# Kernel tuning notes

Measured on AMD Instinct MI355X. Metric: run time of the kernel, lower is better.

Reference implementation:

```python
import jax, jax.numpy as jnp
import numpy as np

N, D, DFF, E, F, K, H = 4096, 512, 512, 512, 4096, 1024, 4


def _rn(i, shape, s=0.02):
    return jax.random.normal(jax.random.fold_in(jax.random.key(0), i), shape, dtype=jnp.float32) * s


def setup_inputs():
    inp = {"inputs": jax.random.normal(jax.random.key(1), (N, D), dtype=jnp.float32)}
    i = 10
    for p in ("enc", "dec"):
        for nm, shp in (("wq", (D, D)), ("wk", (D, D)), ("wv", (D, D)), ("wo", (D, D)), ("w1", (D, DFF)), ("w2", (DFF, D))):
            inp[p + "_" + nm] = _rn(i, shp); i += 1
        for nm, shp in (("bq", (D,)), ("bk", (D,)), ("bv", (D,)), ("bo", (D,)), ("b1", (DFF,)), ("b2", (D,))):
            inp[p + "_" + nm] = jnp.zeros(shp, jnp.float32)
        inp[p + "_ln1_g"] = jnp.ones((D,), jnp.float32)
        inp[p + "_ln1_b"] = jnp.zeros((D,), jnp.float32)
        inp[p + "_ln2_g"] = jnp.ones((D,), jnp.float32)
        inp[p + "_ln2_b"] = jnp.zeros((D,), jnp.float32)
    inp["fc1_w"] = _rn(100, (D, E))
    inp["fc1_b"] = jnp.zeros((E,), jnp.float32)
    inp["fc2_w"] = _rn(101, (D, F))
    inp["fc2_b"] = jnp.zeros((F,), jnp.float32)
    inp["emb"] = _rn(102, (K, E), s=0.01)
    return inp


def layer_norm(x, g, b, eps=1e-6):
    mu = jnp.mean(x, axis=-1, keepdims=True)
    var = jnp.mean(jnp.square(x - mu), axis=-1, keepdims=True)
    return (x - mu) * jax.lax.rsqrt(var + eps) * g + b


def row_distance(a, b):
    # cosine similarity between rows (sim in [-1,1]; loss maps (sim+1)/2 -> [0,1])
    an = a * jax.lax.rsqrt(jnp.maximum(jnp.sum(a * a, axis=1, keepdims=True), 1e-12))
    bn = b * jax.lax.rsqrt(jnp.maximum(jnp.sum(b * b, axis=1, keepdims=True), 1e-12))
    return an @ bn.T


def nearest_context(feature, context):
    distances = row_distance(feature, context) * -1.0  # [N, K]
    min_ind = jnp.argmin(distances, axis=1)
    one_hot = jax.nn.one_hot(min_ind, context.shape[0], dtype=jnp.float32)  # [N, K]
    rslt = one_hot @ jax.lax.stop_gradient(context)  # [N, E]
    return rslt, one_hot


@jax.custom_vjp
def vq(feature, context):
    return nearest_context(feature, context)[0]


def _vq_fwd(feature, context):
    value, ind = nearest_context(feature, context)
    return value, ind


def _vq_bwd(ind, d_value):
    # straight-through to feature, scatter-add (via one-hot matmul) to codebook
    return d_value, ind.T @ d_value


vq.defvjp(_vq_fwd, _vq_bwd)


def encoder_layer(x, wq, bq, wk, bk, wv, bv, wo, bo, w1, b1, w2, b2, g1, be1, g2, be2):
    n, d = x.shape
    dh = d // H
    q = (x @ wq + bq).reshape(n, H, dh)
    k = (x @ wk + bk).reshape(n, H, dh)
    v = (x @ wv + bv).reshape(n, H, dh)
    scores = jnp.einsum('nhd,mhd->hnm', q, k) / jnp.sqrt(jnp.float32(dh))
    attn = jax.nn.softmax(scores, axis=-1)
    ctx = jnp.einsum('hnm,mhd->nhd', attn, v).reshape(n, d)
    out1 = layer_norm(x + (ctx @ wo + bo), g1, be1)
    ffn = jax.nn.relu(out1 @ w1 + b1) @ w2 + b2
    return layer_norm(out1 + ffn, g2, be2)


def reference(inputs, enc_wq, enc_wk, enc_wv, enc_wo, enc_w1, enc_w2, enc_bq, enc_bk, enc_bv, enc_bo, enc_b1, enc_b2, enc_ln1_g, enc_ln1_b, enc_ln2_g, enc_ln2_b, dec_wq, dec_wk, dec_wv, dec_wo, dec_w1, dec_w2, dec_bq, dec_bk, dec_bv, dec_bo, dec_b1, dec_b2, dec_ln1_g, dec_ln1_b, dec_ln2_g, dec_ln2_b, fc1_w, fc1_b, fc2_w, fc2_b, emb):
    encoded = encoder_layer(inputs, enc_wq, enc_bq, enc_wk, enc_bk, enc_wv, enc_bv, enc_wo, enc_bo, enc_w1, enc_b1, enc_w2, enc_b2, enc_ln1_g, enc_ln1_b, enc_ln2_g, enc_ln2_b)
    encoded = encoded @ fc1_w + fc1_b  # [N, E]
    vq_feat = vq(encoded, emb)
    _, context_ind = nearest_context(encoded, emb)
    decoded = encoder_layer(vq_feat, dec_wq, dec_bq, dec_wk, dec_bk, dec_wv, dec_bv, dec_wo, dec_bo, dec_w1, dec_b1, dec_w2, dec_b2, dec_ln1_g, dec_ln1_b, dec_ln2_g, dec_ln2_b)
    decoded = jax.nn.relu(decoded @ fc2_w + fc2_b)  # [N, F]
    return encoded, vq_feat, context_ind, decoded, emb
```

## Files before the change

kernel.cpp:

```cpp
#include <hip/hip_runtime.h>
#include <hip/hip_bf16.h>
#include <stdint.h>

typedef __bf16 bf16;
typedef __bf16 bf16x8 __attribute__((ext_vector_type(8)));
typedef float  f32x4v __attribute__((ext_vector_type(4)));

__device__ __forceinline__ void cvt8(const float* v, bf16x8& hh, bf16x8& ll) {
    #pragma unroll
    for (int j = 0; j < 8; j++) {
        bf16 b = (bf16)v[j]; hh[j] = b; ll[j] = (bf16)(v[j] - (float)b);
    }
}

__device__ __forceinline__ float block_reduce_sum256(float v) {
    __shared__ float red[256];
    int tid = threadIdx.x;
    red[tid] = v; __syncthreads();
    #pragma unroll
    for (int s = 128; s > 0; s >>= 1) {
        if (tid < s) red[tid] += red[tid + s];
        __syncthreads();
    }
    float r = red[0]; __syncthreads();
    return r;
}

template<int BMT, bool RELU, bool TRANS, bool BNAT, bool HILO>
__global__ __launch_bounds__(256, 2)
void gemm3(const float* __restrict__ A, const float* __restrict__ B,
           const float* __restrict__ bias, float* __restrict__ C,
           bf16* __restrict__ Chi, bf16* __restrict__ Clo,
           int K, int lda, int ldb, int ldc, float alpha)
{
    constexpr int BN = 128, TK = 32;
    constexpr int RM = BMT / 32;
    __shared__ __align__(16) bf16 Ah[BMT * TK];
    __shared__ __align__(16) bf16 Al[BMT * TK];
    __shared__ __align__(16) bf16 Bh[BN * TK];
    __shared__ __align__(16) bf16 Bl[BN * TK];

    const int tid  = threadIdx.x;
    const int wave = tid >> 6, lane = tid & 63;
    const int wr = wave >> 1, wc = wave & 1;
    const long bm = (long)blockIdx.y * BMT;
    const long bn = (long)blockIdx.x * BN;
    const int fr = lane & 15, fq = lane >> 4;

    f32x4v acc[RM][4] = {};

    for (int k0 = 0; k0 < K; k0 += TK) {
        #pragma unroll
        for (int it = 0; it < BMT / 64; it++) {
            const int c = it * 256 + tid;
            const int r = c >> 2, k8 = c & 3;
            const float* src = A + (bm + r) * (long)lda + k0 + k8 * 8;
            float4 f0 = ((const float4*)src)[0], f1 = ((const float4*)src)[1];
            float v[8] = {f0.x, f0.y, f0.z, f0.w, f1.x, f1.y, f1.z, f1.w};
            bf16x8 hh, ll; cvt8(v, hh, ll);
            *(bf16x8*)&Ah[r * TK + k8 * 8] = hh;
            *(bf16x8*)&Al[r * TK + k8 * 8] = ll;
        }
        if (BNAT) {
            const int col = tid & 127, bkh = (tid >> 7) * 16;
            const float* src = B + (long)(k0 + bkh) * ldb + bn + col;
            float v[16];
            #pragma unroll
            for (int kk = 0; kk < 16; kk++) v[kk] = src[(long)kk * ldb];
            bf16x8 h0, l0, h1, l1; cvt8(v, h0, l0); cvt8(v + 8, h1, l1);
            bf16* hd = &Bh[col * TK + bkh];
            bf16* ld_ = &Bl[col * TK + bkh];
            ((bf16x8*)hd)[0] = h0; ((bf16x8*)hd)[1] = h1;
            ((bf16x8*)ld_)[0] = l0; ((bf16x8*)ld_)[1] = l1;
        } else {
            #pragma unroll
            for (int it = 0; it < 2; it++) {
                const int c = it * 256 + tid;
                const int r = c >> 2, k8 = c & 3;
                const float* src = B + (bn + r) * (long)ldb + k0 + k8 * 8;
                float4 f0 = ((const float4*)src)[0], f1 = ((const float4*)src)[1];
                float v[8] = {f0.x, f0.y, f0.z, f0.w, f1.x, f1.y, f1.z, f1.w};
                bf16x8 hh, ll; cvt8(v, hh, ll);
                *(bf16x8*)&Bh[r * TK + k8 * 8] = hh;
                *(bf16x8*)&Bl[r * TK + k8 * 8] = ll;
            }
        }
        __syncthreads();

        bf16x8 ah[RM], am[RM], bh[4], bm_[4];
        #pragma unroll
        for (int i = 0; i < RM; i++) {
            const int r = (wr * (BMT / 2) + i * 16 + fr) * TK + fq * 8;
            ah[i] = *(const bf16x8*)&Ah[r];
            am[i] = *(const bf16x8*)&Al[r];
        }
        #pragma unroll
        for (int j = 0; j < 4; j++) {
            const int r = (wc * 64 + j * 16 + fr) * TK + fq * 8;
            bh[j] = *(const bf16x8*)&Bh[r];
            bm_[j] = *(const bf16x8*)&Bl[r];
        }
        #pragma unroll
        for (int i = 0; i < RM; i++)
            #pragma unroll
            for (int j = 0; j < 4; j++) {
                acc[i][j] = __builtin_amdgcn_mfma_f32_16x16x32_bf16(am[i], bh[j], acc[i][j], 0, 0, 0);
                acc[i][j] = __builtin_amdgcn_mfma_f32_16x16x32_bf16(ah[i], bm_[j], acc[i][j], 0, 0, 0);
                acc[i][j] = __builtin_amdgcn_mfma_f32_16x16x32_bf16(ah[i], bh[j], acc[i][j], 0, 0, 0);
            }
        __syncthreads();
    }

    #pragma unroll
    for (int i = 0; i < RM; i++) {
        #pragma unroll
        for (int j = 0; j < 4; j++) {
            const long col = bn + wc * 64 + j * 16 + fr;
            const float bv = bias ? bias[col] : 0.f;
            #pragma unroll
            for (int r = 0; r < 4; r++) {
                const long row = bm + wr * (BMT / 2) + i * 16 + fq * 4 + r;
                float v = acc[i][j][r] * alpha + bv;
                if (RELU) v = fmaxf(v, 0.f);
                const long idx = TRANS ? (col * (long)ldc + row) : (row * (long)ldc + col);
                if (HILO) {
                    bf16 hh = (bf16)v;
                    Chi[idx] = hh;
                    Clo[idx] = (bf16)(v - (float)hh);
                } else {
                    C[idx] = v;
                }
            }
        }
    }
}

__global__ __launch_bounds__(256, 2)
void qkv_gemm(const float* __restrict__ X,
              const float* __restrict__ Wq, const float* __restrict__ Wk, const float* __restrict__ Wv,
              const float* __restrict__ Bq, const float* __restrict__ Bk, const float* __restrict__ Bv,
              float* __restrict__ Qo, bf16* __restrict__ Khi, bf16* __restrict__ Klo,
              bf16* __restrict__ Vthi, bf16* __restrict__ Vtlo)
{
    constexpr int TK = 32, D = 512, N = 4096;
    __shared__ __align__(16) bf16 Ah[64 * TK];
    __shared__ __align__(16) bf16 Al[64 * TK];
    __shared__ __align__(16) bf16 Bh[128 * TK];
    __shared__ __align__(16) bf16 Bl[128 * TK];

    const int tid  = threadIdx.x;
    const int wave = tid >> 6, lane = tid & 63;
    const int wr = wave >> 1, wc = wave & 1;
    const int sel = blockIdx.x >> 2, wcol0 = (blockIdx.x & 3) * 128;
    const long bm = (long)blockIdx.y * 64;
    const int fr = lane & 15, fq = lane >> 4;

    const float* W  = sel == 0 ? Wq : (sel == 1 ? Wk : Wv);
    const float* Bb = sel == 0 ? Bq : (sel == 1 ? Bk : Bv);

    f32x4v acc[2][4] = {};

    for (int k0 = 0; k0 < D; k0 += TK) {
        {
            const int r = tid >> 2, k8 = tid & 3;
            const float* src = X + (bm + r) * (long)D + k0 + k8 * 8;
            float4 f0 = ((const float4*)src)[0], f1 = ((const float4*)src)[1];
            float v[8] = {f0.x, f0.y, f0.z, f0.w, f1.x, f1.y, f1.z, f1.w};
            bf16x8 hh, ll; cvt8(v, hh, ll);
            *(bf16x8*)&Ah[r * TK + k8 * 8] = hh;
            *(bf16x8*)&Al[r * TK + k8 * 8] = ll;
        }
        {
            const int col = tid & 127, bkh = (tid >> 7) * 16;
            const float* src = W + (long)(k0 + bkh) * D + wcol0 + col;
            float v[16];
            #pragma unroll
            for (int kk = 0; kk < 16; kk++) v[kk] = src[(long)kk * D];
            bf16x8 h0, l0, h1, l1; cvt8(v, h0, l0); cvt8(v + 8, h1, l1);
            bf16* hd = &Bh[col * TK + bkh];
            bf16* ld_ = &Bl[col * TK + bkh];
            ((bf16x8*)hd)[0] = h0; ((bf16x8*)hd)[1] = h1;
            ((bf16x8*)ld_)[0] = l0; ((bf16x8*)ld_)[1] = l1;
        }
        __syncthreads();

        bf16x8 ah[2], am[2], bh[4], bm_[4];
        #pragma unroll
        for (int i = 0; i < 2; i++) {
            const int r = (wr * 32 + i * 16 + fr) * TK + fq * 8;
            ah[i] = *(const bf16x8*)&Ah[r];
            am[i] = *(const bf16x8*)&Al[r];
        }
        #pragma unroll
        for (int j = 0; j < 4; j++) {
            const int r = (wc * 64 + j * 16 + fr) * TK + fq * 8;
            bh[j] = *(const bf16x8*)&Bh[r];
            bm_[j] = *(const bf16x8*)&Bl[r];
        }
        #pragma unroll
        for (int i = 0; i < 2; i++)
            #pragma unroll
            for (int j = 0; j < 4; j++) {
                acc[i][j] = __builtin_amdgcn_mfma_f32_16x16x32_bf16(am[i], bh[j], acc[i][j], 0, 0, 0);
                acc[i][j] = __builtin_amdgcn_mfma_f32_16x16x32_bf16(ah[i], bm_[j], acc[i][j], 0, 0, 0);
                acc[i][j] = __builtin_amdgcn_mfma_f32_16x16x32_bf16(ah[i], bh[j], acc[i][j], 0, 0, 0);
            }
        __syncthreads();
    }

    #pragma unroll
    for (int i = 0; i < 2; i++) {
        #pragma unroll
        for (int j = 0; j < 4; j++) {
            const int col = wc * 64 + j * 16 + fr;
            const float bv = Bb[wcol0 + col];
            #pragma unroll
            for (int r = 0; r < 4; r++) {
                const long row = bm + wr * 32 + i * 16 + fq * 4 + r;
                const float v = acc[i][j][r] + bv;
                if (sel == 0) {
                    Qo[row * D + wcol0 + col] = v;
                } else {
                    const bf16 hh = (bf16)v;
                    const bf16 ll = (bf16)(v - (float)hh);
                    const long idx = (sel == 1) ? (row * (long)D + wcol0 + col)
                                                : ((long)(wcol0 + col) * N + row);
                    if (sel == 1) { Khi[idx] = hh; Klo[idx] = ll; }
                    else          { Vthi[idx] = hh; Vtlo[idx] = ll; }
                }
            }
        }
    }
}

__global__ __launch_bounds__(256, 4)
void flash_attn(const float* __restrict__ Q,
                const bf16* __restrict__ Khi, const bf16* __restrict__ Klo,
                const bf16* __restrict__ Vthi, const bf16* __restrict__ Vtlo,
                float* __restrict__ Op, float* __restrict__ ml)
{
    constexpr int N = 4096, D = 512, SPAN = 1024, TKV = 32, NT = SPAN / TKV;
    constexpr float TS = 0.12751791f;

    __shared__ __align__(16) bf16 smem[16384];
    bf16* Kh = smem;
    bf16* Kl = smem + 4096;
    bf16* Vh = smem + 8192;
    bf16* Vl = smem + 12288;

    const int tid = threadIdx.x;
    const int wave = tid >> 6, lane = tid & 63;
    const int fr = lane & 15, fq = lane >> 4;
    const int qt = blockIdx.x, h = blockIdx.y, s = blockIdx.z;
    const long q0 = (long)qt * 64;

    const int kn = tid >> 4, kk8 = tid & 15;
    const int vd = tid >> 2, vk8 = tid & 3;
    const int kof0 = kn * 128 + ((kk8 ^ (kn & 15)) << 3);
    const int kof1 = (kn + 16) * 128 + ((kk8 ^ ((kn + 16) & 15)) << 3);
    const int vof0 = vd * 32 + ((vk8 ^ ((vd >> 2) & 3)) << 3);
    const int vof1 = (vd + 64) * 32 + ((vk8 ^ (((vd + 64) >> 2) & 3)) << 3);

    bf16x8 qh[4], ql[4];
    #pragma unroll
    for (int kt = 0; kt < 4; kt++) {
        const float* src = Q + (q0 + wave * 16 + fr) * D + h * 128 + kt * 32 + fq * 8;
        float4 f0 = ((const float4*)src)[0], f1 = ((const float4*)src)[1];
        float v[8] = {f0.x, f0.y, f0.z, f0.w, f1.x, f1.y, f1.z, f1.w};
        cvt8(v, qh[kt], ql[kt]);
    }

    f32x4v o[8] = {};
    float m_run = -1e30f, l_run = 0.f;

    const int j0base = s * SPAN;

    #pragma unroll 1
    for (int jt = 0; jt < NT; jt++) {
        const int j0 = j0base + jt * TKV;

        {
            const long kg0 = (long)(j0 + kn) * D + h * 128 + kk8 * 8;
            const long kg1 = (long)(j0 + kn + 16) * D + h * 128 + kk8 * 8;
            const long vg0 = (long)(h * 128 + vd) * N + j0 + vk8 * 8;
            const long vg1 = (long)(h * 128 + vd + 64) * N + j0 + vk8 * 8;
            uint4 a0 = *(const uint4*)&Khi[kg0], a1 = *(const uint4*)&Klo[kg0];
            uint4 a2 = *(const uint4*)&Khi[kg1], a3 = *(const uint4*)&Klo[kg1];
            uint4 b0 = *(const uint4*)&Vthi[vg0], b1 = *(const uint4*)&Vtlo[vg0];
            uint4 b2 = *(const uint4*)&Vthi[vg1], b3 = *(const uint4*)&Vtlo[vg1];
            *(uint4*)&Kh[kof0] = a0; *(uint4*)&Kl[kof0] = a1;
            *(uint4*)&Kh[kof1] = a2; *(uint4*)&Kl[kof1] = a3;
            *(uint4*)&Vh[vof0] = b0; *(uint4*)&Vl[vof0] = b1;
            *(uint4*)&Vh[vof1] = b2; *(uint4*)&Vl[vof1] = b3;
        }
        __syncthreads();

        f32x4v sacc[2] = {};
        #pragma unroll
        for (int jb = 0; jb < 2; jb++) {
            bf16x8 kh[4], km[4];
            #pragma unroll
            for (int kt = 0; kt < 4; kt++) {
                const int off = (jb * 16 + fr) * 128 + (((kt * 4 + fq) ^ fr) << 3);
                kh[kt] = *(const bf16x8*)&Kh[off];
                km[kt] = *(const bf16x8*)&Kl[off];
            }
            __builtin_amdgcn_s_setprio(1);
            #pragma unroll
            for (int kt = 0; kt < 4; kt++) {
                sacc[jb] = __builtin_amdgcn_mfma_f32_16x16x32_bf16(km[kt], qh[kt], sacc[jb], 0, 0, 0);
                sacc[jb] = __builtin_amdgcn_mfma_f32_16x16x32_bf16(kh[kt], ql[kt], sacc[jb], 0, 0, 0);
                sacc[jb] = __builtin_amdgcn_mfma_f32_16x16x32_bf16(kh[kt], qh[kt], sacc[jb], 0, 0, 0);
            }
            __builtin_amdgcn_s_setprio(0);
        }

        float t[2][4];
        float mloc = -1e30f;
        #pragma unroll
        for (int jb = 0; jb < 2; jb++)
            #pragma unroll
            for (int r = 0; r < 4; r++) {
                t[jb][r] = sacc[jb][r] * TS;
                mloc = fmaxf(mloc, t[jb][r]);
            }
        mloc = fmaxf(mloc, __shfl_xor(mloc, 16));
        mloc = fmaxf(mloc, __shfl_xor(mloc, 32));
        const float mn = fmaxf(m_run, mloc);
        const float alpha = exp2f(m_run - mn);
        m_run = mn;

        float p[2][4];
        float rs = 0.f;
        #pragma unroll
        for (int jb = 0; jb < 2; jb++)
            #pragma unroll
            for (int r = 0; r < 4; r++) {
                p[jb][r] = exp2f(t[jb][r] - mn);
                rs += p[jb][r];
            }
        rs += __shfl_xor(rs, 16);
        rs += __shfl_xor(rs, 32);
        l_run = l_run * alpha + rs;

        unsigned int hp[2][2], lp[2][2];
        #pragma unroll
        for (int jb = 0; jb < 2; jb++)
            #pragma unroll
            for (int t2 = 0; t2 < 2; t2++) {
                const float p0 = p[jb][2 * t2], p1 = p[jb][2 * t2 + 1];
                const bf16 h0 = (bf16)p0, h1 = (bf16)p1;
                const unsigned short u0 = __builtin_bit_cast(unsigned short, h0);
                const unsigned short u1 = __builtin_bit_cast(unsigned short, h1);
                hp[jb][t2] = (unsigned int)u0 | ((unsigned int)u1 << 16);
                const bf16 g0 = (bf16)(p0 - (float)h0), g1 = (bf16)(p1 - (float)h1);
                const unsigned short w0 = __builtin_bit_cast(unsigned short, g0);
                const unsigned short w1 = __builtin_bit_cast(unsigned short, g1);
                lp[jb][t2] = (unsigned int)w0 | ((unsigned int)w1 << 16);
            }

        uint4 PH, PL;
        {
            unsigned int phw[4], plw[4];
            #pragma unroll
            for (int w = 0; w < 4; w++) {
                const int src = ((2 * (fq & 1) + (w >> 1)) << 4) + fr;
                const unsigned int h0 = (unsigned int)__shfl((int)hp[0][w & 1], src);
                const unsigned int h1 = (unsigned int)__shfl((int)hp[1][w & 1], src);
                phw[w] = (fq >> 1) ? h1 : h0;
                const unsigned int g0 = (unsigned int)__shfl((int)lp[0][w & 1], src);
                const unsigned int g1 = (unsigned int)__shfl((int)lp[1][w & 1], src);
                plw[w] = (fq >> 1) ? g1 : g0;
            }
            PH.x = phw[0]; PH.y = phw[1]; PH.z = phw[2]; PH.w = phw[3];
            PL.x = plw[0]; PL.y = plw[1]; PL.z = plw[2]; PL.w = plw[3];
        }
        const bf16x8 ph = __builtin_bit_cast(bf16x8, PH);
        const bf16x8 pl = __builtin_bit_cast(bf16x8, PL);

        float alr[4];
        #pragma unroll
        for (int r = 0; r < 4; r++) alr[r] = __shfl(alpha, fq * 4 + r);
        #pragma unroll
        for (int jbo = 0; jbo < 8; jbo++)
            #pragma unroll
            for (int r = 0; r < 4; r++)
                o[jbo][r] *= alr[r];

        #pragma unroll
        for (int jbo = 0; jbo < 8; jbo++) {
            const int off = (jbo * 16 + fr) * 32 + ((fq ^ ((fr >> 2) & 3)) << 3);
            const bf16x8 vh_ = *(const bf16x8*)&Vh[off];
            const bf16x8 vl_ = *(const bf16x8*)&Vl[off];
            __builtin_amdgcn_s_setprio(1);
            o[jbo] = __builtin_amdgcn_mfma_f32_16x16x32_bf16(pl, vh_, o[jbo], 0, 0, 0);
            o[jbo] = __builtin_amdgcn_mfma_f32_16x16x32_bf16(ph, vl_, o[jbo], 0, 0, 0);
            o[jbo] = __builtin_amdgcn_mfma_f32_16x16x32_bf16(ph, vh_, o[jbo], 0, 0, 0);
            __builtin_amdgcn_s_setprio(0);
        }
        __syncthreads();
    }

    const long sidx = (long)((h * 64 + qt) * 4 + s);
    float* ob = Op + sidx * 8192;
    #pragma unroll
    for (int jbo = 0; jbo < 8; jbo++)
        #pragma unroll
        for (int r = 0; r < 4; r++) {
            const int lrow = wave * 16 + fq * 4 + r;
            ob[lrow * 128 + jbo * 16 + fr] = o[jbo][r];
        }
    if (fq == 0) {
        const int lrow = wave * 16 + fr;
        ml[sidx * 128 + lrow]      = m_run;
        ml[sidx * 128 + 64 + lrow] = l_run;
    }
}

__global__ void flash_merge(const float* __restrict__ Op, const float* __restrict__ ml,
                            float* __restrict__ ctx)
{
    const int idx = blockIdx.x;
    const int h = idx >> 6, qt = idx & 63;
    const int tid = threadIdx.x;
    __shared__ float es[4][64], il[64];
    if (tid < 64) {
        float m[4], l[4];
        #pragma unroll
        for (int s = 0; s < 4; s++) {
            m[s] = ml[(long)(idx * 4 + s) * 128 + tid];
            l[s] = ml[(long)(idx * 4 + s) * 128 + 64 + tid];
        }
        float mx = fmaxf(fmaxf(m[0], m[1]), fmaxf(m[2], m[3]));
        float denom = 0.f;
        #pragma unroll
        for (int s = 0; s < 4; s++) {
            const float e = exp2f(m[s] - mx);
            es[s][tid] = e;
            denom += e * l[s];
        }
        il[tid] = 1.f / denom;
    }
    __syncthreads();
    const long b = (long)idx * 4 * 8192;
    #pragma unroll
    for (int i = 0; i < 32; i++) {
        const int e = tid + i * 256;
        const int row = e >> 7, col = e & 127;
        float v = es[0][row] * Op[b + e] + es[1][row] * Op[b + 8192 + e]
                + es[2][row] * Op[b + 16384 + e] + es[3][row] * Op[b + 24576 + e];
        ctx[(long)(qt * 64 + row) * 512 + h * 128 + col] = v * il[row];
    }
}

__global__ void add_ln_f32(const float* __restrict__ a, const float* __restrict__ b,
                           const float* __restrict__ g, const float* __restrict__ be,
                           float* __restrict__ out)
{
    const long row = blockIdx.x;
    const int tid = threadIdx.x;
    const long base = row * 512L;
    float x0 = a[base + tid]       + b[base + tid];
    float x1 = a[base + tid + 256] + b[base + tid + 256];
    float s = block_reduce_sum256(x0 + x1);
    float mu = s * (1.f / 512.f);
    float d0 = x0 - mu, d1 = x1 - mu;
    float var = block_reduce_sum256(d0 * d0 + d1 * d1) * (1.f / 512.f);
    float invs = rsqrtf(var + 1e-6f);
    out[base + tid]       = d0 * invs * g[tid]       + be[tid];
    out[base + tid + 256] = d1 * invs * g[tid + 256] + be[tid + 256];
}

__global__ void normalize_emb(const float* __restrict__ emb, float* __restrict__ embn)
{
    const long row = blockIdx.x;
    const int tid = threadIdx.x;
    const long base = row * 512L;
    float a0 = emb[base + tid];
    float a1 = emb[base + tid + 256];
    float ss = block_reduce_sum256(a0 * a0 + a1 * a1);
    float sc = rsqrtf(fmaxf(ss, 1e-12f));
    embn[base + tid]       = a0 * sc;
    embn[base + tid + 256] = a1 * sc;
}

__global__ void vq_select_onehot(float* __restrict__ sims, const float* __restrict__ emb,
                                 float* __restrict__ vq_out)
{
    __shared__ float sv[256];
    __shared__ int   si[256];
    const long row = blockIdx.x;
    const int tid = threadIdx.x;
    float* s = sims + row * 1024L;
    float v0 = s[tid], v1 = s[tid + 256], v2 = s[tid + 512], v3 = s[tid + 768];
    float best = v0; int bi = tid;
    if (v1 > best) { best = v1; bi = tid + 256; }
    if (v2 > best) { best = v2; bi = tid + 512; }
    if (v3 > best) { best = v3; bi = tid + 768; }
    sv[tid] = best; si[tid] = bi; __syncthreads();
    #pragma unroll
    for (int st = 128; st > 0; st >>= 1) {
        if (tid < st) {
            if (sv[tid + st] > sv[tid] ||
                (sv[tid + st] == sv[tid] && si[tid + st] < si[tid])) {
                sv[tid] = sv[tid + st]; si[tid] = si[tid + st];
            }
        }
        __syncthreads();
    }
    const int idx = si[0];
    s[tid]       = (tid       == idx) ? 1.f : 0.f;
    s[tid + 256] = (tid + 256 == idx) ? 1.f : 0.f;
    s[tid + 512] = (tid + 512 == idx) ? 1.f : 0.f;
    s[tid + 768] = (tid + 768 == idx) ? 1.f : 0.f;
    const float* er = emb + (long)idx * 512;
    float* vr = vq_out + row * 512L;
    vr[tid]       = er[tid];
    vr[tid + 256] = er[tid + 256];
}

struct EncW {
    const float *wq, *wk, *wv, *wo, *w1, *w2;
    const float *bq, *bk, *bv, *bo, *b1, *b2;
    const float *g1, *be1, *g2, *be2;
};

static void run_encoder_g3(hipStream_t stream, const float* x, const EncW& w,
                           float* qb, bf16* khi, bf16* klo, bf16* vthi, bf16* vtlo,
                           float* ctx, float* Op, float* ml,
                           float* x1, float* hb, float* out)
{
    const int N = 4096, D = 512;
    qkv_gemm<<<dim3(12, 64), 256, 0, stream>>>(
        x, w.wq, w.wk, w.wv, w.bq, w.bk, w.bv, qb, khi, klo, vthi, vtlo);
    flash_attn<<<dim3(64, 4, 4), 256, 0, stream>>>(qb, khi, klo, vthi, vtlo, Op, ml);
    flash_merge<<<256, 256, 0, stream>>>(Op, ml, ctx);
    gemm3<64, false, false, true, false><<<dim3(4, 64), 256, 0, stream>>>(
        ctx, w.wo, w.bo, qb, nullptr, nullptr, D, D, D, D, 1.f);
    add_ln_f32<<<N, 256, 0, stream>>>(x, qb, w.g1, w.be1, x1);
    gemm3<64, true, false, true, false><<<dim3(4, 64), 256, 0, stream>>>(
        x1, w.w1, w.b1, hb, nullptr, nullptr, D, D, D, D, 1.f);
    gemm3<64, false, false, true, false><<<dim3(4, 64), 256, 0, stream>>>(
        hb, w.w2, w.b2, qb, nullptr, nullptr, D, D, D, D, 1.f);
    add_ln_f32<<<N, 256, 0, stream>>>(x1, qb, w.g2, w.be2, out);
}

extern "C" void kernel_launch(void* const* d_in, const int* in_sizes, int n_in,
                              void* d_out, int out_size, void* d_ws, size_t ws_size,
                              hipStream_t stream)
{
    const int N = 4096, D = 512, E = 512, F = 4096, KCB = 1024;
    (void)in_sizes; (void)n_in; (void)out_size; (void)d_ws; (void)ws_size;

    const float* x_in  = (const float*)d_in[0];
    const float* fc1_w = (const float*)d_in[33];
    const float* fc1_b = (const float*)d_in[34];
    const float* fc2_w = (const float*)d_in[35];
    const float* fc2_b = (const float*)d_in[36];
    const float* emb   = (const float*)d_in[37];

    float* out0 = (float*)d_out;
    float* out1 = out0 + (size_t)N * E;
    float* out2 = out1 + (size_t)N * E;
    float* out3 = out2 + (size_t)N * KCB;
    float* out4 = out3 + (size_t)N * F;

    char* arena = (char*)out3;
    const size_t MB = 1024 * 1024;
    float* qb     = (float*)(arena + 0 * MB);
    bf16*  khi    = (bf16*) (arena + 8 * MB);
    bf16*  klo    = (bf16*) (arena + 12 * MB);
    bf16*  vthi   = (bf16*) (arena + 16 * MB);
    bf16*  vtlo   = (bf16*) (arena + 20 * MB);
    float* ctx    = (float*)(arena + 24 * MB);
    float* Op     = (float*)(arena + 32 * MB);
    float* decout = (float*)(arena + 56 * MB);
    float* x1     = (float*)(arena + 16 * MB);
    float* hb     = (float*)(arena + 8 * MB);
    float* ml     = (float*)out4;
    float* embn   = out1;
    float* stage  = (float*)out4;

    EncW ew = { (const float*)d_in[1],  (const float*)d_in[2],  (const float*)d_in[3],
                (const float*)d_in[4],  (const float*)d_in[5],  (const float*)d_in[6],
                (const float*)d_in[7],  (const float*)d_in[8],  (const float*)d_in[9],
                (const float*)d_in[10], (const float*)d_in[11], (const float*)d_in[12],
                (const float*)d_in[13], (const float*)d_in[14], (const float*)d_in[15],
                (const float*)d_in[16] };
    EncW dw = { (const float*)d_in[17], (const float*)d_in[18], (const float*)d_in[19],
                (const float*)d_in[20], (const float*)d_in[21], (const float*)d_in[22],
                (const float*)d_in[23], (const float*)d_in[24], (const float*)d_in[25],
                (const float*)d_in[26], (const float*)d_in[27], (const float*)d_in[28],
                (const float*)d_in[29], (const float*)d_in[30], (const float*)d_in[31],
                (const float*)d_in[32] };

    normalize_emb<<<KCB, 256, 0, stream>>>(emb, embn);
    run_encoder_g3(stream, x_in, ew, qb, khi, klo, vthi, vtlo, ctx, Op, ml, x1, hb, ctx);

    gemm3<64, false, false, true, false><<<dim3(4, 64), 256, 0, stream>>>(
        ctx, fc1_w, fc1_b, out0, nullptr, nullptr, D, D, E, E, 1.f);

    gemm3<128, false, false, false, false><<<dim3(8, 32), 256, 0, stream>>>(
        out0, embn, nullptr, out2, nullptr, nullptr, E, E, E, KCB, 1.f);
    vq_select_onehot<<<N, 256, 0, stream>>>(out2, emb, out1);

    run_encoder_g3(stream, out1, dw, qb, khi, klo, vthi, vtlo, ctx, Op, ml, x1, hb, decout);

    hipMemcpyAsync(stage, decout + (size_t)3584 * D, (size_t)512 * D * sizeof(float),
                   hipMemcpyDeviceToDevice, stream);
    gemm3<128, true, false, true, false><<<dim3(F / 128, 3584 / 128), 256, 0, stream>>>(
        decout, fc2_w, fc2_b, out3, nullptr, nullptr, D, D, F, F, 1.f);
    gemm3<128, true, false, true, false><<<dim3(F / 128, 512 / 128), 256, 0, stream>>>(
        stage, fc2_w, fc2_b, out3 + (size_t)3584 * F, nullptr, nullptr, D, D, F, F, 1.f);

    hipMemcpyAsync(out4, emb, (size_t)KCB * E * sizeof(float), hipMemcpyDeviceToDevice, stream);
}
```

Baseline: 920.6 us.

## Give each flash-attention wave two query row groups, halving block threads

The flash attention kernel now runs 2 waves per block instead of 4, and each wave handles 32 query rows as two 16-row groups. Each K/V fragment read from shared memory then feeds MFMAs for both groups, which halves LDS reads per unit of MFMA work. Each thread also does twice the global-to-shared staging. Register pressure roughly doubles (Q fragments, accumulators, softmax state), and the grid stays the same, so there are fewer waves in flight overall.

```diff
diff --git a/kernel.cpp b/kernel.cpp
--- a/kernel.cpp
+++ b/kernel.cpp
@@ -233,7 +233,7 @@
     }
 }
 
-__global__ __launch_bounds__(256, 4)
+__global__ __launch_bounds__(128, 2)
 void flash_attn(const float* __restrict__ Q,
                 const bf16* __restrict__ Khi, const bf16* __restrict__ Klo,
                 const bf16* __restrict__ Vthi, const bf16* __restrict__ Vtlo,
@@ -256,22 +256,20 @@
 
     const int kn = tid >> 4, kk8 = tid & 15;
     const int vd = tid >> 2, vk8 = tid & 3;
-    const int kof0 = kn * 128 + ((kk8 ^ (kn & 15)) << 3);
-    const int kof1 = (kn + 16) * 128 + ((kk8 ^ ((kn + 16) & 15)) << 3);
-    const int vof0 = vd * 32 + ((vk8 ^ ((vd >> 2) & 3)) << 3);
-    const int vof1 = (vd + 64) * 32 + ((vk8 ^ (((vd + 64) >> 2) & 3)) << 3);
-
-    bf16x8 qh[4], ql[4];
-    #pragma unroll
-    for (int kt = 0; kt < 4; kt++) {
-        const float* src = Q + (q0 + wave * 16 + fr) * D + h * 128 + kt * 32 + fq * 8;
-        float4 f0 = ((const float4*)src)[0], f1 = ((const float4*)src)[1];
-        float v[8] = {f0.x, f0.y, f0.z, f0.w, f1.x, f1.y, f1.z, f1.w};
-        cvt8(v, qh[kt], ql[kt]);
-    }
-
-    f32x4v o[8] = {};
-    float m_run = -1e30f, l_run = 0.f;
+
+    bf16x8 qh[2][4], ql[2][4];
+    #pragma unroll
+    for (int rg = 0; rg < 2; rg++)
+        #pragma unroll
+        for (int kt = 0; kt < 4; kt++) {
+            const float* src = Q + (q0 + wave * 32 + rg * 16 + fr) * D + h * 128 + kt * 32 + fq * 8;
+            float4 f0 = ((const float4*)src)[0], f1 = ((const float4*)src)[1];
+            float v[8] = {f0.x, f0.y, f0.z, f0.w, f1.x, f1.y, f1.z, f1.w};
+            cvt8(v, qh[rg][kt], ql[rg][kt]);
+        }
+
+    f32x4v o[2][8] = {};
+    float m_run[2] = {-1e30f, -1e30f}, l_run[2] = {0.f, 0.f};
 
     const int j0base = s * SPAN;
 
@@ -279,23 +277,22 @@
     for (int jt = 0; jt < NT; jt++) {
         const int j0 = j0base + jt * TKV;
 
-        {
-            const long kg0 = (long)(j0 + kn) * D + h * 128 + kk8 * 8;
-            const long kg1 = (long)(j0 + kn + 16) * D + h * 128 + kk8 * 8;
-            const long vg0 = (long)(h * 128 + vd) * N + j0 + vk8 * 8;
-            const long vg1 = (long)(h * 128 + vd + 64) * N + j0 + vk8 * 8;
-            uint4 a0 = *(const uint4*)&Khi[kg0], a1 = *(const uint4*)&Klo[kg0];
-            uint4 a2 = *(const uint4*)&Khi[kg1], a3 = *(const uint4*)&Klo[kg1];
-            uint4 b0 = *(const uint4*)&Vthi[vg0], b1 = *(const uint4*)&Vtlo[vg0];
-            uint4 b2 = *(const uint4*)&Vthi[vg1], b3 = *(const uint4*)&Vtlo[vg1];
-            *(uint4*)&Kh[kof0] = a0; *(uint4*)&Kl[kof0] = a1;
-            *(uint4*)&Kh[kof1] = a2; *(uint4*)&Kl[kof1] = a3;
-            *(uint4*)&Vh[vof0] = b0; *(uint4*)&Vl[vof0] = b1;
-            *(uint4*)&Vh[vof1] = b2; *(uint4*)&Vl[vof1] = b3;
-        }
-        __syncthreads();
-
-        f32x4v sacc[2] = {};
+        #pragma unroll
+        for (int i = 0; i < 4; i++) {
+            const int n = kn + 8 * i;
+            const long kg = (long)(j0 + n) * D + h * 128 + kk8 * 8;
+            const int ko = n * 128 + ((kk8 ^ (n & 15)) << 3);
+            *(uint4*)&Kh[ko] = *(const uint4*)&Khi[kg];
+            *(uint4*)&Kl[ko] = *(const uint4*)&Klo[kg];
+            const int d = vd + 32 * i;
+            const long vg = (long)(h * 128 + d) * N + j0 + vk8 * 8;
+            const int vo = d * 32 + ((vk8 ^ ((d >> 2) & 3)) << 3);
+            *(uint4*)&Vh[vo] = *(const uint4*)&Vthi[vg];
+            *(uint4*)&Vl[vo] = *(const uint4*)&Vtlo[vg];
+        }
+        __syncthreads();
+
+        f32x4v sacc[2][2] = {};
         #pragma unroll
         for (int jb = 0; jb < 2; jb++) {
             bf16x8 kh[4], km[4];
@@ -307,85 +304,95 @@
             }
             __builtin_amdgcn_s_setprio(1);
             #pragma unroll
-            for (int kt = 0; kt < 4; kt++) {
-                sacc[jb] = __builtin_amdgcn_mfma_f32_16x16x32_bf16(km[kt], qh[kt], sacc[jb], 0, 0, 0);
-                sacc[jb] = __builtin_amdgcn_mfma_f32_16x16x32_bf16(kh[kt], ql[kt], sacc[jb], 0, 0, 0);
-                sacc[jb] = __builtin_amdgcn_mfma_f32_16x16x32_bf16(kh[kt], qh[kt], sacc[jb], 0, 0, 0);
-            }
+            for (int kt = 0; kt < 4; kt++)
+                #pragma unroll
+                for (int rg = 0; rg < 2; rg++) {
+                    sacc[rg][jb] = __builtin_amdgcn_mfma_f32_16x16x32_bf16(km[kt], qh[rg][kt], sacc[rg][jb], 0, 0, 0);
+                    sacc[rg][jb] = __builtin_amdgcn_mfma_f32_16x16x32_bf16(kh[kt], ql[rg][kt], sacc[rg][jb], 0, 0, 0);
+                    sacc[rg][jb] = __builtin_amdgcn_mfma_f32_16x16x32_bf16(kh[kt], qh[rg][kt], sacc[rg][jb], 0, 0, 0);
+                }
             __builtin_amdgcn_s_setprio(0);
         }
 
-        float t[2][4];
-        float mloc = -1e30f;
-        #pragma unroll
-        for (int jb = 0; jb < 2; jb++)
-            #pragma unroll
-            for (int r = 0; r < 4; r++) {
-                t[jb][r] = sacc[jb][r] * TS;
-                mloc = fmaxf(mloc, t[jb][r]);
-            }
-        mloc = fmaxf(mloc, __shfl_xor(mloc, 16));
-        mloc = fmaxf(mloc, __shfl_xor(mloc, 32));
-        const float mn = fmaxf(m_run, mloc);
-        const float alpha = exp2f(m_run - mn);
-        m_run = mn;
-
-        float p[2][4];
-        float rs = 0.f;
-        #pragma unroll
-        for (int jb = 0; jb < 2; jb++)
-            #pragma unroll
-            for (int r = 0; r < 4; r++) {
-                p[jb][r] = exp2f(t[jb][r] - mn);
-                rs += p[jb][r];
-            }
-        rs += __shfl_xor(rs, 16);
-        rs += __shfl_xor(rs, 32);
-        l_run = l_run * alpha + rs;
-
-        unsigned int hp[2][2], lp[2][2];
-        #pragma unroll
-        for (int jb = 0; jb < 2; jb++)
-            #pragma unroll
-            for (int t2 = 0; t2 < 2; t2++) {
-                const float p0 = p[jb][2 * t2], p1 = p[jb][2 * t2 + 1];
-                const bf16 h0 = (bf16)p0, h1 = (bf16)p1;
-                const unsigned short u0 = __builtin_bit_cast(unsigned short, h0);
-                const unsigned short u1 = __builtin_bit_cast(unsigned short, h1);
-                hp[jb][t2] = (unsigned int)u0 | ((unsigned int)u1 << 16);
-                const bf16 g0 = (bf16)(p0 - (float)h0), g1 = (bf16)(p1 - (float)h1);
-                const unsigned short w0 = __builtin_bit_cast(unsigned short, g0);
-                const unsigned short w1 = __builtin_bit_cast(unsigned short, g1);
-                lp[jb][t2] = (unsigned int)w0 | ((unsigned int)w1 << 16);
-            }
-
-        uint4 PH, PL;
-        {
-            unsigned int phw[4], plw[4];
-            #pragma unroll
-            for (int w = 0; w < 4; w++) {
-                const int src = ((2 * (fq & 1) + (w >> 1)) << 4) + fr;
-                const unsigned int h0 = (unsigned int)__shfl((int)hp[0][w & 1], src);
-                const unsigned int h1 = (unsigned int)__shfl((int)hp[1][w & 1], src);
-                phw[w] = (fq >> 1) ? h1 : h0;
-                const unsigned int g0 = (unsigned int)__shfl((int)lp[0][w & 1], src);
-                const unsigned int g1 = (unsigned int)__shfl((int)lp[1][w & 1], src);
-                plw[w] = (fq >> 1) ? g1 : g0;
-            }
-            PH.x = phw[0]; PH.y = phw[1]; PH.z = phw[2]; PH.w = phw[3];
-            PL.x = plw[0]; PL.y = plw[1]; PL.z = plw[2]; PL.w = plw[3];
-        }
-        const bf16x8 ph = __builtin_bit_cast(bf16x8, PH);
-        const bf16x8 pl = __builtin_bit_cast(bf16x8, PL);
-
-        float alr[4];
-        #pragma unroll
-        for (int r = 0; r < 4; r++) alr[r] = __shfl(alpha, fq * 4 + r);
-        #pragma unroll
-        for (int jbo = 0; jbo < 8; jbo++)
-            #pragma unroll
-            for (int r = 0; r < 4; r++)
-                o[jbo][r] *= alr[r];
+        bf16x8 ph[2], pl[2];
+        float alpha[2];
+        #pragma unroll
+        for (int rg = 0; rg < 2; rg++) {
+            float t[2][4];
+            float mloc = -1e30f;
+            #pragma unroll
+            for (int jb = 0; jb < 2; jb++)
+                #pragma unroll
+                for (int r = 0; r < 4; r++) {
+                    t[jb][r] = sacc[rg][jb][r] * TS;
+                    mloc = fmaxf(mloc, t[jb][r]);
+                }
+            mloc = fmaxf(mloc, __shfl_xor(mloc, 16));
+            mloc = fmaxf(mloc, __shfl_xor(mloc, 32));
+            const float mn = fmaxf(m_run[rg], mloc);
+            alpha[rg] = exp2f(m_run[rg] - mn);
+            m_run[rg] = mn;
+
+            float p[2][4];
+            float rs = 0.f;
+            #pragma unroll
+            for (int jb = 0; jb < 2; jb++)
+                #pragma unroll
+                for (int r = 0; r < 4; r++) {
+                    p[jb][r] = exp2f(t[jb][r] - mn);
+                    rs += p[jb][r];
+                }
+            rs += __shfl_xor(rs, 16);
+            rs += __shfl_xor(rs, 32);
+            l_run[rg] = l_run[rg] * alpha[rg] + rs;
+
+            unsigned int hp[2][2], lp[2][2];
+            #pragma unroll
+            for (int jb = 0; jb < 2; jb++)
+                #pragma unroll
+                for (int t2 = 0; t2 < 2; t2++) {
+                    const float p0 = p[jb][2 * t2], p1 = p[jb][2 * t2 + 1];
+                    const bf16 h0 = (bf16)p0, h1 = (bf16)p1;
+                    const unsigned short u0 = __builtin_bit_cast(unsigned short, h0);
+                    const unsigned short u1 = __builtin_bit_cast(unsigned short, h1);
+                    hp[jb][t2] = (unsigned int)u0 | ((unsigned int)u1 << 16);
+                    const bf16 g0 = (bf16)(p0 - (float)h0), g1 = (bf16)(p1 - (float)h1);
+                    const unsigned short w0 = __builtin_bit_cast(unsigned short, g0);
+                    const unsigned short w1 = __builtin_bit_cast(unsigned short, g1);
+                    lp[jb][t2] = (unsigned int)w0 | ((unsigned int)w1 << 16);
+                }
+
+            uint4 PH, PL;
+            {
+                unsigned int phw[4], plw[4];
+                #pragma unroll
+                for (int w = 0; w < 4; w++) {
+                    const int src = ((2 * (fq & 1) + (w >> 1)) << 4) + fr;
+                    const unsigned int h0 = (unsigned int)__shfl((int)hp[0][w & 1], src);
+                    const unsigned int h1 = (unsigned int)__shfl((int)hp[1][w & 1], src);
+                    phw[w] = (fq >> 1) ? h1 : h0;
+                    const unsigned int g0 = (unsigned int)__shfl((int)lp[0][w & 1], src);
+                    const unsigned int g1 = (unsigned int)__shfl((int)lp[1][w & 1], src);
+                    plw[w] = (fq >> 1) ? g1 : g0;
+                }
+                PH.x = phw[0]; PH.y = phw[1]; PH.z = phw[2]; PH.w = phw[3];
+                PL.x = plw[0]; PL.y = plw[1]; PL.z = plw[2]; PL.w = plw[3];
+            }
+            ph[rg] = __builtin_bit_cast(bf16x8, PH);
+            pl[rg] = __builtin_bit_cast(bf16x8, PL);
+        }
+
+        #pragma unroll
+        for (int rg = 0; rg < 2; rg++) {
+            float alr[4];
+            #pragma unroll
+            for (int r = 0; r < 4; r++) alr[r] = __shfl(alpha[rg], fq * 4 + r);
+            #pragma unroll
+            for (int jbo = 0; jbo < 8; jbo++)
+                #pragma unroll
+                for (int r = 0; r < 4; r++)
+                    o[rg][jbo][r] *= alr[r];
+        }
 
         #pragma unroll
         for (int jbo = 0; jbo < 8; jbo++) {
@@ -393,9 +400,12 @@
             const bf16x8 vh_ = *(const bf16x8*)&Vh[off];
             const bf16x8 vl_ = *(const bf16x8*)&Vl[off];
             __builtin_amdgcn_s_setprio(1);
-            o[jbo] = __builtin_amdgcn_mfma_f32_16x16x32_bf16(pl, vh_, o[jbo], 0, 0, 0);
-            o[jbo] = __builtin_amdgcn_mfma_f32_16x16x32_bf16(ph, vl_, o[jbo], 0, 0, 0);
-            o[jbo] = __builtin_amdgcn_mfma_f32_16x16x32_bf16(ph, vh_, o[jbo], 0, 0, 0);
+            #pragma unroll
+            for (int rg = 0; rg < 2; rg++) {
+                o[rg][jbo] = __builtin_amdgcn_mfma_f32_16x16x32_bf16(pl[rg], vh_, o[rg][jbo], 0, 0, 0);
+                o[rg][jbo] = __builtin_amdgcn_mfma_f32_16x16x32_bf16(ph[rg], vl_, o[rg][jbo], 0, 0, 0);
+                o[rg][jbo] = __builtin_amdgcn_mfma_f32_16x16x32_bf16(ph[rg], vh_, o[rg][jbo], 0, 0, 0);
+            }
             __builtin_amdgcn_s_setprio(0);
         }
         __syncthreads();
@@ -404,16 +414,21 @@
     const long sidx = (long)((h * 64 + qt) * 4 + s);
     float* ob = Op + sidx * 8192;
     #pragma unroll
-    for (int jbo = 0; jbo < 8; jbo++)
-        #pragma unroll
-        for (int r = 0; r < 4; r++) {
-            const int lrow = wave * 16 + fq * 4 + r;
-            ob[lrow * 128 + jbo * 16 + fr] = o[jbo][r];
-        }
+    for (int rg = 0; rg < 2; rg++)
+        #pragma unroll
+        for (int jbo = 0; jbo < 8; jbo++)
+            #pragma unroll
+            for (int r = 0; r < 4; r++) {
+                const int lrow = wave * 32 + rg * 16 + fq * 4 + r;
+                ob[lrow * 128 + jbo * 16 + fr] = o[rg][jbo][r];
+            }
     if (fq == 0) {
-        const int lrow = wave * 16 + fr;
-        ml[sidx * 128 + lrow]      = m_run;
-        ml[sidx * 128 + 64 + lrow] = l_run;
+        #pragma unroll
+        for (int rg = 0; rg < 2; rg++) {
+            const int lrow = wave * 32 + rg * 16 + fr;
+            ml[sidx * 128 + lrow]      = m_run[rg];
+            ml[sidx * 128 + 64 + lrow] = l_run[rg];
+        }
     }
 }
 
@@ -533,7 +548,7 @@
     const int N = 4096, D = 512;
     qkv_gemm<<<dim3(12, 64), 256, 0, stream>>>(
         x, w.wq, w.wk, w.wv, w.bq, w.bk, w.bv, qb, khi, klo, vthi, vtlo);
-    flash_attn<<<dim3(64, 4, 4), 256, 0, stream>>>(qb, khi, klo, vthi, vtlo, Op, ml);
+    flash_attn<<<dim3(64, 4, 4), 128, 0, stream>>>(qb, khi, klo, vthi, vtlo, Op, ml);
     flash_merge<<<256, 256, 0, stream>>>(Op, ml, ctx);
     gemm3<64, false, false, true, false><<<dim3(4, 64), 256, 0, stream>>>(
         ctx, w.wo, w.bo, qb, nullptr, nullptr, D, D, D, D, 1.f);
```

Result: faster. 897.0 us (-2.6%).
